# Kernel optimization log

Measured on AMD Instinct MI355X. Metric: run time of the kernel, lower is better.

The kernel has to match this reference:

```python
import jax, jax.numpy as jnp
import numpy as np
from jax import lax

ALPHA = 0.2                       # LeakyReLU leakage
BN_SCALE = 1.0 / np.sqrt(1.0 + 1e-3)  # inference-mode BN with default stats (mean=0, var=1, eps=1e-3)
COEFF = np.array([[-1., 3., -3., 1.],
                  [3., -6., 3., 0.],
                  [-3., 0., 3., 0.],
                  [1., 4., 1., 0.]], dtype=np.float32)


def _conv(x, w):
    return lax.conv_general_dilated(x, w, (1, 1), 'SAME',
                                    dimension_numbers=('NHWC', 'HWIO', 'NHWC'))


def _lrelu(x):
    return jnp.where(x > 0, x, ALPHA * x)


def _avgpool2(x):
    b, h, w, c = x.shape
    return x.reshape(b, h // 2, 2, w // 2, 2, c).mean(axis=(2, 4))


def _run_cnn(fixed, moving, ws, fw0, fw1, pw0, pw1):
    x = jnp.concatenate([fixed, moving], axis=-1)  # [B,H,W,2]
    for w in ws:
        x = _avgpool2(_lrelu(BN_SCALE * _conv(x, w)))
    x = _lrelu(BN_SCALE * _conv(x, fw0))
    x = _lrelu(BN_SCALE * _conv(x, fw1))
    x = _lrelu(_conv(x, pw0))
    return _conv(x, pw1)  # [B, H/2^s, W/2^s, 2] coarse displacements


def _range_grid(n, size):
    # mirrors __makeMeshgrids: step = 1/floor(size/n), clipped to [0, n-1]
    fd = size // n
    step = 1.0 / fd
    r = np.arange(0.0, n + step * (fd - 1), step)[:size]
    return np.clip(r, 0.0, n - 1).astype(np.float32)


def _bvec(t):
    return jnp.stack([t ** 3, t ** 2, t, jnp.ones_like(t)], axis=-1)


def _bspline_interp(disp, H, W):
    ny, nx = disp.shape[1], disp.shape[2]
    xr = _range_grid(nx, W)
    yr = _range_grid(ny, H)
    xx, yy = np.meshgrid(xr, yr)               # [H, W]
    ii = np.floor(xx).astype(np.int32)
    jj = np.floor(yy).astype(np.int32)
    u = jnp.asarray((xx / nx).astype(np.float32))
    v = jnp.asarray((yy / ny).astype(np.float32))
    padded = jnp.pad(disp, ((0, 0), (1, 3), (1, 3), (0, 0)))
    # G[m, n, b, h, w, c] = padded[b, jj+m, ii+n, c]  (m ~ add_j, n ~ add_i)
    G = jnp.stack([jnp.stack([padded[:, jj + m, ii + n, :] for n in range(4)], 0)
                   for m in range(4)], 0)
    B_u = jnp.einsum('hwk,kl->hwl', _bvec(u), jnp.asarray(COEFF))
    B_v = jnp.einsum('hwk,kl->hwl', _bvec(v), jnp.asarray(COEFF))
    # matches: interm_u = B_u . m-axis ; res = interm_u . B_v over n-axis
    return jnp.einsum('hwm,hwn,mnbhwc->bhwc', B_u, B_v, G)


def _bilinear(img, wx, wy, H, W):
    eps = 1e-5
    x0 = jnp.clip(jnp.floor(wx), 0, W - 1)
    x1 = jnp.clip(jnp.floor(wx) + 1, 0, W - 1)
    y0 = jnp.clip(jnp.floor(wy), 0, H - 1)
    y1 = jnp.clip(jnp.floor(wy) + 1, 0, H - 1)
    x0i = x0.astype(jnp.int32); x1i = x1.astype(jnp.int32)
    y0i = y0.astype(jnp.int32); y1i = y1.astype(jnp.int32)
    im = img[..., 0]                            # [B,H,W], channel 0 only
    b = jnp.arange(im.shape[0])[:, None, None]
    Q1 = im[b, y0i, x0i]
    Q2 = im[b, y1i, x0i]
    Q3 = im[b, y0i, x1i]
    Q4 = im[b, y1i, x1i]
    wxr = (x1 - wx) / (x1 - x0 + eps)
    wxl = (wx - x0) / (x1 - x0 + eps)
    R1 = wxr * Q1 + wxl * Q3
    R2 = wxr * Q2 + wxl * Q4
    out = (y1 - wy) / (y1 - y0 + eps) * R1 + (wy - y0) / (y1 - y0 + eps) * R2
    return out[..., None]                       # [B,H,W,1]


def _forward(fixed, moving, w0, w1, w2, fw0, fw1, pw0, pw1):
    B, H, W, _ = moving.shape
    disp = _run_cnn(fixed, moving, (w0, w1, w2), fw0, fw1, pw0, pw1)
    interp = _bspline_interp(disp, H, W)        # [B,H,W,2]
    gx, gy = np.meshgrid(np.arange(W, dtype=np.float32), np.arange(H, dtype=np.float32))
    wx = interp[..., 0] + gx                    # warped x coords
    wy = interp[..., 1] + gy                    # warped y coords
    warped = _bilinear(moving, wx, wy, H, W)
    warped_grid = jnp.stack([wx, wy], axis=1)   # [B,2,H,W]
    return warped, warped_grid


def setup_inputs() -> dict:
    key = jax.random.key(0)
    ks = jax.random.split(key, 9)
    B, H, W = 4, 512, 512
    s = 0.05
    return {
        'fixed':  jax.random.normal(ks[0], (B, H, W, 1), jnp.float32),
        'moving': jax.random.normal(ks[1], (B, H, W, 1), jnp.float32),
        'w0':  s * jax.random.normal(ks[2], (3, 3, 2, 32), jnp.float32),
        'w1':  s * jax.random.normal(ks[3], (3, 3, 32, 32), jnp.float32),
        'w2':  s * jax.random.normal(ks[4], (3, 3, 32, 32), jnp.float32),
        'fw0': s * jax.random.normal(ks[5], (3, 3, 32, 32), jnp.float32),
        'fw1': s * jax.random.normal(ks[6], (3, 3, 32, 32), jnp.float32),
        'pw0': s * jax.random.normal(ks[7], (1, 1, 32, 32), jnp.float32),
        'pw1': s * jax.random.normal(ks[8], (1, 1, 32, 2), jnp.float32),
    }


def reference(fixed, moving, w0, w1, w2, fw0, fw1, pw0, pw1):
    return _forward(fixed, moving, w0, w1, w2, fw0, fw1, pw0, pw1)
```

## Files before the change

kernel.cpp:

```cpp
#include <hip/hip_runtime.h>
#include <hip/hip_bf16.h>

typedef __hip_bfloat16 bf16;
typedef __attribute__((ext_vector_type(8))) short s8v;
typedef __attribute__((ext_vector_type(16))) float f16v;

#define BNS 0.9995003746877732f

__device__ __forceinline__ float lrelu(float x) { return x > 0.f ? x : 0.2f * x; }

struct b4 { bf16 a, b, c, d; };
__device__ __forceinline__ float4 load4(const bf16* p) {
    const b4 q = *reinterpret_cast<const b4*>(p);
    return make_float4(__bfloat162float(q.a), __bfloat162float(q.b),
                       __bfloat162float(q.c), __bfloat162float(q.d));
}

__global__ __launch_bounds__(256) void k_repack(const float* __restrict__ wa,
                                                const float* __restrict__ wb,
                                                const float* __restrict__ wc,
                                                const float* __restrict__ wd,
                                                const float* __restrict__ w0,
                                                bf16* __restrict__ wf)
{
    const int idx = blockIdx.x * 256 + threadIdx.x;
    if (idx < 36864) {
        const int layer = idx / 9216;
        const int r = idx - layer * 9216;
        const int j = r & 7;
        const int l = (r >> 3) & 63;
        const int t = r >> 9;
        const int k = t * 16 + ((l >> 5) << 3) + j;
        const int tap = k >> 5, ci = k & 31, co = l & 31;
        const float* W = layer == 0 ? wa : layer == 1 ? wb : layer == 2 ? wc : wd;
        wf[idx] = __float2bfloat16(W[(tap * 32 + ci) * 32 + co]);
    } else {
        const int r = idx - 36864;
        const int j = r & 7;
        const int l = (r >> 3) & 63;
        const int s = r >> 9;
        const int k = s * 16 + ((l >> 5) << 3) + j;
        const int co = l & 31;
        const float v = (k < 18) ? w0[(k >> 1) * 64 + (k & 1) * 32 + co] : 0.f;
        wf[idx] = __float2bfloat16(v);
    }
}

__global__ __launch_bounds__(256) void k_stage0_mfma(const float* __restrict__ fx,
                                                     const float* __restrict__ mv,
                                                     const bf16* __restrict__ wf,
                                                     bf16* __restrict__ out)
{
    __shared__ uint lds[180];
    const int tid  = threadIdx.x;
    const int lane = tid & 63;
    const int wv   = tid >> 6;
    const int x0 = blockIdx.x * 16;
    const int y0 = blockIdx.y * 8;
    const int b  = blockIdx.z;

    if (tid < 180) {
        const int row = tid / 18, col = tid - row * 18;
        const int gy = y0 - 1 + row, gx = x0 - 1 + col;
        float vf = 0.f, vm = 0.f;
        if ((unsigned)gy < 512u && (unsigned)gx < 512u) {
            const size_t idx = ((size_t)b * 512 + gy) * 512 + gx;
            vf = fx[idx]; vm = mv[idx];
        }
        union { bf16 h[2]; uint u; } pk;
        pk.h[0] = __float2bfloat16(vf);
        pk.h[1] = __float2bfloat16(vm);
        lds[tid] = pk.u;
    }
    __syncthreads();

    const int m  = lane & 31;
    const int h  = lane >> 5;
    const int dy = m >> 4;
    const int xx = m & 15;
    const int rbase = 2 * wv + dy;

    uint p[16];
#pragma unroll
    for (int i = 9; i < 16; ++i) p[i] = 0u;
#pragma unroll
    for (int ky = 0; ky < 3; ++ky)
#pragma unroll
        for (int kx = 0; kx < 3; ++kx)
            p[ky * 3 + kx] = lds[(rbase + ky) * 18 + xx + kx];

    f16v acc;
#pragma unroll
    for (int i = 0; i < 16; ++i) acc[i] = 0.f;

#pragma unroll
    for (int s = 0; s < 2; ++s) {
        union { uint u[4]; s8v v; } af;
#pragma unroll
        for (int q = 0; q < 4; ++q) af.u[q] = p[s * 8 + h * 4 + q];
        const s8v bfg = *reinterpret_cast<const s8v*>(&wf[(s * 64 + lane) * 8]);
        acc = __builtin_amdgcn_mfma_f32_32x32x16_bf16(af.v, bfg, acc, 0, 0, 0);
    }

    const int co = lane & 31;
    const int prow = blockIdx.y * 4 + wv;
#pragma unroll
    for (int q = 0; q < 4; ++q) {
        const int base = ((q & 1) << 1) + ((q >> 1) << 2);
        const float s = lrelu(BNS * acc[base])     + lrelu(BNS * acc[base + 1])
                      + lrelu(BNS * acc[base + 8]) + lrelu(BNS * acc[base + 9]);
        const int c = (q & 1) + 2 * h + ((q >> 1) << 2);
        out[(((size_t)b * 256 + prow) * 256 + (blockIdx.x * 8 + c)) * 32 + co] =
            __float2bfloat16(0.25f * s);
    }
}

template <bool POOL>
__global__ __launch_bounds__(256) void k_conv_mfma(const bf16* __restrict__ in,
                                                   const bf16* __restrict__ wf,
                                                   bf16* __restrict__ out,
                                                   int Hi, int Wi)
{
    __shared__ __align__(16) short lds[7200];
    const int tid  = threadIdx.x;
    const int lane = tid & 63;
    const int wv   = tid >> 6;
    const int x0 = blockIdx.x * 16;
    const int y0 = blockIdx.y * 8;
    const int b  = blockIdx.z;

    for (int i = tid; i < 1440; i += 256) {
        const int c4 = i & 7;
        const int p  = i >> 3;
        const int row = p / 18, col = p - row * 18;
        const int gy = y0 - 1 + row, gx = x0 - 1 + col;
        uint2 v = make_uint2(0u, 0u);
        if ((unsigned)gy < (unsigned)Hi && (unsigned)gx < (unsigned)Wi)
            v = *reinterpret_cast<const uint2*>(&in[(((size_t)b * Hi + gy) * Wi + gx) * 32 + c4 * 4]);
        *reinterpret_cast<uint2*>(&lds[p * 40 + c4 * 4]) = v;
    }
    __syncthreads();

    const int m  = lane & 31;
    const int h  = lane >> 5;
    const int dy = m >> 4;
    const int xx = m & 15;
    const int rbase = 2 * wv + dy;

    f16v acc;
#pragma unroll
    for (int i = 0; i < 16; ++i) acc[i] = 0.f;

#pragma unroll
    for (int t = 0; t < 18; ++t) {
        const int tap = t >> 1;
        const int ky = tap / 3, kx = tap % 3;
        const int ci_ofs = ((t & 1) << 4) + (h << 3);
        const s8v a = *reinterpret_cast<const s8v*>(
            &lds[((rbase + ky) * 18 + (xx + kx)) * 40 + ci_ofs]);
        const s8v bf = *reinterpret_cast<const s8v*>(&wf[(t * 64 + lane) * 8]);
        acc = __builtin_amdgcn_mfma_f32_32x32x16_bf16(a, bf, acc, 0, 0, 0);
    }

    const int co = lane & 31;
    if (POOL) {
        const int Ho = Hi >> 1, Wo = Wi >> 1;
        const int prow = blockIdx.y * 4 + wv;
#pragma unroll
        for (int q = 0; q < 4; ++q) {
            const int base = ((q & 1) << 1) + ((q >> 1) << 2);
            const float s = lrelu(BNS * acc[base])     + lrelu(BNS * acc[base + 1])
                          + lrelu(BNS * acc[base + 8]) + lrelu(BNS * acc[base + 9]);
            const int c = (q & 1) + 2 * h + ((q >> 1) << 2);
            out[(((size_t)b * Ho + prow) * Wo + (blockIdx.x * 8 + c)) * 32 + co] =
                __float2bfloat16(0.25f * s);
        }
    } else {
#pragma unroll
        for (int r = 0; r < 16; ++r) {
            const int mm = (r & 3) + ((r >> 2) << 3) + (h << 2);
            const int gy = y0 + 2 * wv + (mm >> 4);
            const int gx = x0 + (mm & 15);
            out[(((size_t)b * Hi + gy) * Wi + gx) * 32 + co] =
                __float2bfloat16(lrelu(BNS * acc[r]));
        }
    }
}

__global__ __launch_bounds__(256) void k_pw(const bf16* __restrict__ in,
                                            const float* __restrict__ pw0,
                                            const float* __restrict__ pw1,
                                            float* __restrict__ disp)
{
    __shared__ float w0t[1024];
    __shared__ float w1s[64];
    const int tid = threadIdx.x;
    for (int i = tid; i < 1024; i += 256) {
        const int ci = i >> 5, co = i & 31;
        w0t[co * 32 + ci] = pw0[i];
    }
    if (tid < 64) w1s[tid] = pw1[tid];
    __syncthreads();

    const int p = blockIdx.x * 256 + tid;
    float4 iv[8];
#pragma unroll
    for (int g = 0; g < 8; ++g)
        iv[g] = load4(&in[(size_t)p * 32 + g * 4]);

    float d0 = 0.f, d1 = 0.f;
#pragma unroll 4
    for (int co = 0; co < 32; ++co) {
        float s = 0.f;
#pragma unroll
        for (int g = 0; g < 8; ++g) {
            const float4 wv = *reinterpret_cast<const float4*>(&w0t[co * 32 + g * 4]);
            s += iv[g].x * wv.x + iv[g].y * wv.y + iv[g].z * wv.z + iv[g].w * wv.w;
        }
        const float p0 = lrelu(s);
        d0 += p0 * w1s[co * 2 + 0];
        d1 += p0 * w1s[co * 2 + 1];
    }
    disp[(size_t)p * 2 + 0] = d0;
    disp[(size_t)p * 2 + 1] = d1;
}

__global__ __launch_bounds__(256) void k_warp(const float* __restrict__ disp,
                                              const float* __restrict__ mv,
                                              float* __restrict__ out)
{
    const int idx = blockIdx.x * 256 + threadIdx.x;
    const int b = idx >> 18;
    const int h = (idx >> 9) & 511;
    const int w = idx & 511;

    const float xg = fminf(w * 0.125f, 63.0f);
    const float yg = fminf(h * 0.125f, 63.0f);
    const int ii = w >> 3, jj = h >> 3;
    const float u = xg * 0.015625f, v = yg * 0.015625f;

    const float u2 = u * u, u3 = u2 * u;
    const float v2 = v * v, v3 = v2 * v;
    const float Bu[4] = {-u3 + 3.f * u2 - 3.f * u + 1.f,
                         3.f * u3 - 6.f * u2 + 4.f,
                         -3.f * u3 + 3.f * u2 + 3.f * u + 1.f,
                         u3};
    const float Bv[4] = {-v3 + 3.f * v2 - 3.f * v + 1.f,
                         3.f * v3 - 6.f * v2 + 4.f,
                         -3.f * v3 + 3.f * v2 + 3.f * v + 1.f,
                         v3};

    float s0 = 0.f, s1 = 0.f;
#pragma unroll
    for (int m = 0; m < 4; ++m) {
        const int gy = jj + m - 1;
        float r0 = 0.f, r1 = 0.f;
        if ((unsigned)gy < 64u) {
#pragma unroll
            for (int n = 0; n < 4; ++n) {
                const int gx = ii + n - 1;
                if ((unsigned)gx < 64u) {
                    const size_t di = (((size_t)b * 64 + gy) * 64 + gx) * 2;
                    r0 += Bv[n] * disp[di];
                    r1 += Bv[n] * disp[di + 1];
                }
            }
        }
        s0 += Bu[m] * r0;
        s1 += Bu[m] * r1;
    }
    const float wx = s0 + (float)w;
    const float wy = s1 + (float)h;

    const float fx = floorf(wx), fy = floorf(wy);
    const float x0 = fminf(fmaxf(fx, 0.f), 511.f);
    const float x1 = fminf(fmaxf(fx + 1.f, 0.f), 511.f);
    const float y0 = fminf(fmaxf(fy, 0.f), 511.f);
    const float y1 = fminf(fmaxf(fy + 1.f, 0.f), 511.f);
    const int x0i = (int)x0, x1i = (int)x1, y0i = (int)y0, y1i = (int)y1;

    float ov;
    if (x0i == x1i || y0i == y1i) {
        ov = 0.f;
    } else {
        const size_t bb = (size_t)b * 262144;
        const float Q1 = mv[bb + (size_t)y0i * 512 + x0i];
        const float Q2 = mv[bb + (size_t)y1i * 512 + x0i];
        const float Q3 = mv[bb + (size_t)y0i * 512 + x1i];
        const float Q4 = mv[bb + (size_t)y1i * 512 + x1i];
        const float invdx = 1.f / (x1 - x0 + 1e-5f);
        const float wxr = (x1 - wx) * invdx, wxl = (wx - x0) * invdx;
        const float R1 = wxr * Q1 + wxl * Q3;
        const float R2 = wxr * Q2 + wxl * Q4;
        const float invdy = 1.f / (y1 - y0 + 1e-5f);
        ov = (y1 - wy) * invdy * R1 + (wy - y0) * invdy * R2;
    }

    out[idx] = ov;
    const size_t gbase = 1048576;
    out[gbase + (size_t)(b * 2 + 0) * 262144 + (size_t)h * 512 + w] = wx;
    out[gbase + (size_t)(b * 2 + 1) * 262144 + (size_t)h * 512 + w] = wy;
}

extern "C" void kernel_launch(void* const* d_in, const int* in_sizes, int n_in,
                              void* d_out, int out_size, void* d_ws, size_t ws_size,
                              hipStream_t stream) {
    (void)in_sizes; (void)n_in; (void)out_size; (void)ws_size;
    const float* fixed  = (const float*)d_in[0];
    const float* moving = (const float*)d_in[1];
    const float* w0  = (const float*)d_in[2];
    const float* w1  = (const float*)d_in[3];
    const float* w2  = (const float*)d_in[4];
    const float* fw0 = (const float*)d_in[5];
    const float* fw1 = (const float*)d_in[6];
    const float* pw0 = (const float*)d_in[7];
    const float* pw1 = (const float*)d_in[8];

    char* base = (char*)d_ws;
    bf16*  a0  = (bf16*)base;
    bf16*  a1  = (bf16*)(base + (16u << 20));
    bf16*  a2  = (bf16*)base;
    bf16*  f0  = (bf16*)(base + (1u << 20));
    bf16*  f1  = (bf16*)(base + (2u << 20));
    float* dsp = (float*)(base + (3u << 20));
    bf16*  wfr = (bf16*)d_out;

    k_repack<<<148, 256, 0, stream>>>(w1, w2, fw0, fw1, w0, wfr);
    k_stage0_mfma<<<dim3(32, 64, 4), 256, 0, stream>>>(fixed, moving, wfr + 36864, a0);
    k_conv_mfma<true ><<<dim3(16, 32, 4), 256, 0, stream>>>(a0, wfr + 0 * 9216, a1, 256, 256);
    k_conv_mfma<true ><<<dim3( 8, 16, 4), 256, 0, stream>>>(a1, wfr + 1 * 9216, a2, 128, 128);
    k_conv_mfma<false><<<dim3( 4,  8, 4), 256, 0, stream>>>(a2, wfr + 2 * 9216, f0,  64,  64);
    k_conv_mfma<false><<<dim3( 4,  8, 4), 256, 0, stream>>>(f0, wfr + 3 * 9216, f1,  64,  64);
    k_pw<<<64, 256, 0, stream>>>(f1, pw0, pw1, dsp);
    k_warp<<<4096, 256, 0, stream>>>(dsp, moving, (float*)d_out);
}
```

Measured before the change: 146.6 us.

## Fuse conv stages into front and tail kernels with halo recompute in LDS

Merges stage-0 conv with the first pooled conv into one kernel that computes the 256x256 intermediate tile (with halo) in shared memory, skipping the global round-trip of the largest activation. Also fuses the two 64x64 convs, the pointwise head, and the B-spline warp into a single tail kernel that keeps per-tile displacements in LDS. Launch count drops from eight to four. In exchange, halo regions are recomputed redundantly, and the tail runs only 256 blocks with heavy LDS use, which may limit occupancy.

```diff
diff --git a/kernel.cpp b/kernel.cpp
--- a/kernel.cpp
+++ b/kernel.cpp
@@ -14,6 +14,25 @@
     const b4 q = *reinterpret_cast<const b4*>(p);
     return make_float4(__bfloat162float(q.a), __bfloat162float(q.b),
                        __bfloat162float(q.c), __bfloat162float(q.d));
+}
+
+__device__ __forceinline__ f16v conv18(const short* lds, int ldw, int pi, int pj,
+                                       int h, const bf16* __restrict__ wf, int lane)
+{
+    f16v acc;
+#pragma unroll
+    for (int i = 0; i < 16; ++i) acc[i] = 0.f;
+#pragma unroll
+    for (int t = 0; t < 18; ++t) {
+        const int tap = t >> 1;
+        const int ky = tap / 3, kx = tap % 3;
+        const int ci_ofs = ((t & 1) << 4) + (h << 3);
+        const s8v a = *reinterpret_cast<const s8v*>(
+            &lds[((pi + ky) * ldw + (pj + kx)) * 40 + ci_ofs]);
+        const s8v bfg = *reinterpret_cast<const s8v*>(&wf[(t * 64 + lane) * 8]);
+        acc = __builtin_amdgcn_mfma_f32_32x32x16_bf16(a, bfg, acc, 0, 0, 0);
+    }
+    return acc;
 }
 
 __global__ __launch_bounds__(256) void k_repack(const float* __restrict__ wa,
@@ -46,63 +65,83 @@
     }
 }
 
-__global__ __launch_bounds__(256) void k_stage0_mfma(const float* __restrict__ fx,
-                                                     const float* __restrict__ mv,
-                                                     const bf16* __restrict__ wf,
-                                                     bf16* __restrict__ out)
+__global__ __launch_bounds__(256) void k_front(const float* __restrict__ fx,
+                                               const float* __restrict__ mv,
+                                               const bf16* __restrict__ wfs0,
+                                               const bf16* __restrict__ wfc1,
+                                               bf16* __restrict__ a1)
 {
-    __shared__ uint lds[180];
+    __shared__ uint rawL[864];
+    __shared__ __align__(16) short a0L[7200];
     const int tid  = threadIdx.x;
     const int lane = tid & 63;
     const int wv   = tid >> 6;
+    const int h  = lane >> 5;
+    const int m  = lane & 31;
+    const int dy = m >> 4;
+    const int xx = m & 15;
     const int x0 = blockIdx.x * 16;
     const int y0 = blockIdx.y * 8;
     const int b  = blockIdx.z;
-
-    if (tid < 180) {
-        const int row = tid / 18, col = tid - row * 18;
-        const int gy = y0 - 1 + row, gx = x0 - 1 + col;
-        float vf = 0.f, vm = 0.f;
-        if ((unsigned)gy < 512u && (unsigned)gx < 512u) {
-            const size_t idx = ((size_t)b * 512 + gy) * 512 + gx;
-            vf = fx[idx]; vm = mv[idx];
-        }
-        union { bf16 h[2]; uint u; } pk;
-        pk.h[0] = __float2bfloat16(vf);
-        pk.h[1] = __float2bfloat16(vm);
-        lds[tid] = pk.u;
-    }
-    __syncthreads();
-
-    const int m  = lane & 31;
-    const int h  = lane >> 5;
-    const int dy = m >> 4;
-    const int xx = m & 15;
-    const int rbase = 2 * wv + dy;
-
-    uint p[16];
-#pragma unroll
-    for (int i = 9; i < 16; ++i) p[i] = 0u;
-#pragma unroll
-    for (int ky = 0; ky < 3; ++ky)
-#pragma unroll
-        for (int kx = 0; kx < 3; ++kx)
-            p[ky * 3 + kx] = lds[(rbase + ky) * 18 + xx + kx];
-
-    f16v acc;
-#pragma unroll
-    for (int i = 0; i < 16; ++i) acc[i] = 0.f;
-
-#pragma unroll
-    for (int s = 0; s < 2; ++s) {
-        union { uint u[4]; s8v v; } af;
-#pragma unroll
-        for (int q = 0; q < 4; ++q) af.u[q] = p[s * 8 + h * 4 + q];
-        const s8v bfg = *reinterpret_cast<const s8v*>(&wf[(s * 64 + lane) * 8]);
-        acc = __builtin_amdgcn_mfma_f32_32x32x16_bf16(af.v, bfg, acc, 0, 0, 0);
-    }
-
     const int co = lane & 31;
+
+    for (int i = tid; i < 864; i += 256) {
+        uint pk = 0u;
+        if (i < 836) {
+            const int row = i / 38, col = i - (i / 38) * 38;
+            const int gy = 2 * y0 - 3 + row, gx = 2 * x0 - 3 + col;
+            if ((unsigned)gy < 512u && (unsigned)gx < 512u) {
+                const size_t idx = ((size_t)b * 512 + gy) * 512 + gx;
+                union { bf16 hh[2]; uint u; } p;
+                p.hh[0] = __float2bfloat16(fx[idx]);
+                p.hh[1] = __float2bfloat16(mv[idx]);
+                pk = p.u;
+            }
+        }
+        rawL[i] = pk;
+    }
+    __syncthreads();
+
+    const s8v b0 = *reinterpret_cast<const s8v*>(&wfs0[(0 * 64 + lane) * 8]);
+    const s8v b1 = *reinterpret_cast<const s8v*>(&wfs0[(1 * 64 + lane) * 8]);
+    for (int T = wv; T < 30; T += 4) {
+        const int r = T / 3, g = T - 3 * r;
+        const int pr = 2 * r + dy, pc = g * 16 + xx;
+        uint p[9];
+#pragma unroll
+        for (int ky = 0; ky < 3; ++ky)
+#pragma unroll
+            for (int kx = 0; kx < 3; ++kx)
+                p[ky * 3 + kx] = rawL[(pr + ky) * 38 + pc + kx];
+
+        f16v acc;
+#pragma unroll
+        for (int i = 0; i < 16; ++i) acc[i] = 0.f;
+        union { uint u[4]; s8v v; } a0f, a1f;
+#pragma unroll
+        for (int q = 0; q < 4; ++q) a0f.u[q] = p[h * 4 + q];
+        a1f.u[0] = (h == 0) ? p[8] : 0u;
+        a1f.u[1] = 0u; a1f.u[2] = 0u; a1f.u[3] = 0u;
+        acc = __builtin_amdgcn_mfma_f32_32x32x16_bf16(a0f.v, b0, acc, 0, 0, 0);
+        acc = __builtin_amdgcn_mfma_f32_32x32x16_bf16(a1f.v, b1, acc, 0, 0, 0);
+
+#pragma unroll
+        for (int q = 0; q < 4; ++q) {
+            const int base = ((q & 1) << 1) + ((q >> 1) << 2);
+            const float s = lrelu(BNS * acc[base])     + lrelu(BNS * acc[base + 1])
+                          + lrelu(BNS * acc[base + 8]) + lrelu(BNS * acc[base + 9]);
+            const int col = g * 8 + ((q & 1) + 2 * h + ((q >> 1) << 2));
+            if (col < 18) {
+                const int gy0 = y0 - 1 + r, gx0 = x0 - 1 + col;
+                const float val = ((unsigned)gy0 < 256u && (unsigned)gx0 < 256u)
+                                  ? 0.25f * s : 0.f;
+                a0L[(r * 18 + col) * 40 + co] = __float2bfloat16(val);
+            }
+        }
+    }
+    __syncthreads();
+
+    const f16v acc = conv18(a0L, 18, 2 * wv + dy, xx, h, wfc1, lane);
     const int prow = blockIdx.y * 4 + wv;
 #pragma unroll
     for (int q = 0; q < 4; ++q) {
@@ -110,16 +149,15 @@
         const float s = lrelu(BNS * acc[base])     + lrelu(BNS * acc[base + 1])
                       + lrelu(BNS * acc[base + 8]) + lrelu(BNS * acc[base + 9]);
         const int c = (q & 1) + 2 * h + ((q >> 1) << 2);
-        out[(((size_t)b * 256 + prow) * 256 + (blockIdx.x * 8 + c)) * 32 + co] =
+        a1[(((size_t)b * 128 + prow) * 128 + (blockIdx.x * 8 + c)) * 32 + co] =
             __float2bfloat16(0.25f * s);
     }
 }
 
-template <bool POOL>
-__global__ __launch_bounds__(256) void k_conv_mfma(const bf16* __restrict__ in,
-                                                   const bf16* __restrict__ wf,
-                                                   bf16* __restrict__ out,
-                                                   int Hi, int Wi)
+__global__ __launch_bounds__(256) void k_conv2(const bf16* __restrict__ in,
+                                               const bf16* __restrict__ wf,
+                                               bf16* __restrict__ out,
+                                               int Hi, int Wi)
 {
     __shared__ __align__(16) short lds[7200];
     const int tid  = threadIdx.x;
@@ -145,161 +183,197 @@
     const int h  = lane >> 5;
     const int dy = m >> 4;
     const int xx = m & 15;
-    const int rbase = 2 * wv + dy;
-
-    f16v acc;
-#pragma unroll
-    for (int i = 0; i < 16; ++i) acc[i] = 0.f;
-
-#pragma unroll
-    for (int t = 0; t < 18; ++t) {
-        const int tap = t >> 1;
-        const int ky = tap / 3, kx = tap % 3;
-        const int ci_ofs = ((t & 1) << 4) + (h << 3);
-        const s8v a = *reinterpret_cast<const s8v*>(
-            &lds[((rbase + ky) * 18 + (xx + kx)) * 40 + ci_ofs]);
-        const s8v bf = *reinterpret_cast<const s8v*>(&wf[(t * 64 + lane) * 8]);
-        acc = __builtin_amdgcn_mfma_f32_32x32x16_bf16(a, bf, acc, 0, 0, 0);
-    }
+
+    const f16v acc = conv18(lds, 18, 2 * wv + dy, xx, h, wf, lane);
 
     const int co = lane & 31;
-    if (POOL) {
-        const int Ho = Hi >> 1, Wo = Wi >> 1;
-        const int prow = blockIdx.y * 4 + wv;
-#pragma unroll
-        for (int q = 0; q < 4; ++q) {
-            const int base = ((q & 1) << 1) + ((q >> 1) << 2);
-            const float s = lrelu(BNS * acc[base])     + lrelu(BNS * acc[base + 1])
-                          + lrelu(BNS * acc[base + 8]) + lrelu(BNS * acc[base + 9]);
-            const int c = (q & 1) + 2 * h + ((q >> 1) << 2);
-            out[(((size_t)b * Ho + prow) * Wo + (blockIdx.x * 8 + c)) * 32 + co] =
-                __float2bfloat16(0.25f * s);
-        }
-    } else {
-#pragma unroll
-        for (int r = 0; r < 16; ++r) {
-            const int mm = (r & 3) + ((r >> 2) << 3) + (h << 2);
-            const int gy = y0 + 2 * wv + (mm >> 4);
-            const int gx = x0 + (mm & 15);
-            out[(((size_t)b * Hi + gy) * Wi + gx) * 32 + co] =
-                __float2bfloat16(lrelu(BNS * acc[r]));
-        }
-    }
-}
-
-__global__ __launch_bounds__(256) void k_pw(const bf16* __restrict__ in,
-                                            const float* __restrict__ pw0,
-                                            const float* __restrict__ pw1,
-                                            float* __restrict__ disp)
-{
-    __shared__ float w0t[1024];
-    __shared__ float w1s[64];
-    const int tid = threadIdx.x;
-    for (int i = tid; i < 1024; i += 256) {
-        const int ci = i >> 5, co = i & 31;
-        w0t[co * 32 + ci] = pw0[i];
-    }
-    if (tid < 64) w1s[tid] = pw1[tid];
-    __syncthreads();
-
-    const int p = blockIdx.x * 256 + tid;
-    float4 iv[8];
-#pragma unroll
-    for (int g = 0; g < 8; ++g)
-        iv[g] = load4(&in[(size_t)p * 32 + g * 4]);
-
-    float d0 = 0.f, d1 = 0.f;
-#pragma unroll 4
-    for (int co = 0; co < 32; ++co) {
-        float s = 0.f;
-#pragma unroll
-        for (int g = 0; g < 8; ++g) {
-            const float4 wv = *reinterpret_cast<const float4*>(&w0t[co * 32 + g * 4]);
-            s += iv[g].x * wv.x + iv[g].y * wv.y + iv[g].z * wv.z + iv[g].w * wv.w;
-        }
-        const float p0 = lrelu(s);
-        d0 += p0 * w1s[co * 2 + 0];
-        d1 += p0 * w1s[co * 2 + 1];
-    }
-    disp[(size_t)p * 2 + 0] = d0;
-    disp[(size_t)p * 2 + 1] = d1;
-}
-
-__global__ __launch_bounds__(256) void k_warp(const float* __restrict__ disp,
+    const int Ho = Hi >> 1, Wo = Wi >> 1;
+    const int prow = blockIdx.y * 4 + wv;
+#pragma unroll
+    for (int q = 0; q < 4; ++q) {
+        const int base = ((q & 1) << 1) + ((q >> 1) << 2);
+        const float s = lrelu(BNS * acc[base])     + lrelu(BNS * acc[base + 1])
+                      + lrelu(BNS * acc[base + 8]) + lrelu(BNS * acc[base + 9]);
+        const int c = (q & 1) + 2 * h + ((q >> 1) << 2);
+        out[(((size_t)b * Ho + prow) * Wo + (blockIdx.x * 8 + c)) * 32 + co] =
+            __float2bfloat16(0.25f * s);
+    }
+}
+
+__global__ __launch_bounds__(256) void k_tail(const bf16* __restrict__ a2,
+                                              const bf16* __restrict__ wf2,
+                                              const bf16* __restrict__ wf3,
+                                              const float* __restrict__ pw0,
+                                              const float* __restrict__ pw1,
                                               const float* __restrict__ mv,
                                               float* __restrict__ out)
 {
-    const int idx = blockIdx.x * 256 + threadIdx.x;
-    const int b = idx >> 18;
-    const int h = (idx >> 9) & 511;
-    const int w = idx & 511;
-
-    const float xg = fminf(w * 0.125f, 63.0f);
-    const float yg = fminf(h * 0.125f, 63.0f);
-    const int ii = w >> 3, jj = h >> 3;
-    const float u = xg * 0.015625f, v = yg * 0.015625f;
-
-    const float u2 = u * u, u3 = u2 * u;
-    const float v2 = v * v, v3 = v2 * v;
-    const float Bu[4] = {-u3 + 3.f * u2 - 3.f * u + 1.f,
-                         3.f * u3 - 6.f * u2 + 4.f,
-                         -3.f * u3 + 3.f * u2 + 3.f * u + 1.f,
-                         u3};
-    const float Bv[4] = {-v3 + 3.f * v2 - 3.f * v + 1.f,
-                         3.f * v3 - 6.f * v2 + 4.f,
-                         -3.f * v3 + 3.f * v2 + 3.f * v + 1.f,
-                         v3};
-
-    float s0 = 0.f, s1 = 0.f;
-#pragma unroll
-    for (int m = 0; m < 4; ++m) {
-        const int gy = jj + m - 1;
-        float r0 = 0.f, r1 = 0.f;
-        if ((unsigned)gy < 64u) {
-#pragma unroll
-            for (int n = 0; n < 4; ++n) {
-                const int gx = ii + n - 1;
-                if ((unsigned)gx < 64u) {
-                    const size_t di = (((size_t)b * 64 + gy) * 64 + gx) * 2;
-                    r0 += Bv[n] * disp[di];
-                    r1 += Bv[n] * disp[di + 1];
+    __shared__ __align__(16) short a2L[288 * 40];
+    __shared__ __align__(16) short f0L[252 * 40];
+    __shared__ __align__(16) short f1L[121 * 40];
+    __shared__ float dspL[121 * 2];
+    __shared__ float w0t[1024];
+    __shared__ float w1s[64];
+
+    const int tid  = threadIdx.x;
+    const int lane = tid & 63;
+    const int wv   = tid >> 6;
+    const int h  = lane >> 5;
+    const int dy = (lane & 31) >> 4;
+    const int xx = lane & 15;
+    const int co = lane & 31;
+    const int bx = blockIdx.x, by = blockIdx.y, b = blockIdx.z;
+    const int Dy = by * 8 - 1, Dx = bx * 8 - 1;
+
+    for (int i = tid; i < 2304; i += 256) {
+        const int c4 = i & 7;
+        const int p  = i >> 3;
+        const int row = p / 18, col = p - row * 18;
+        const int gy = Dy - 2 + row, gx = Dx - 2 + col;
+        uint2 v = make_uint2(0u, 0u);
+        if (row < 15 && col < 15 && (unsigned)gy < 64u && (unsigned)gx < 64u)
+            v = *reinterpret_cast<const uint2*>(&a2[(((size_t)b * 64 + gy) * 64 + gx) * 32 + c4 * 4]);
+        *reinterpret_cast<uint2*>(&a2L[p * 40 + c4 * 4]) = v;
+    }
+    for (int i = tid; i < 560; i += 256) {
+        const int p28 = i / 20, w = i - (i / 20) * 20;
+        const int row = p28 >> 1, col = 16 + (p28 & 1);
+        reinterpret_cast<uint*>(f0L)[(row * 18 + col) * 20 + w] = 0u;
+    }
+    for (int i = tid; i < 1024; i += 256) {
+        const int ci = i >> 5, c = i & 31;
+        w0t[c * 32 + ci] = pw0[i];
+    }
+    if (tid < 64) w1s[tid] = pw1[tid];
+    __syncthreads();
+
+    for (int T = wv; T < 7; T += 4) {
+        const f16v acc = conv18(a2L, 18, 2 * T + dy, xx, h, wf2, lane);
+#pragma unroll
+        for (int r = 0; r < 16; ++r) {
+            const int row32 = (r & 3) + ((r >> 2) << 3) + (h << 2);
+            const int i = 2 * T + (row32 >> 4);
+            const int j = row32 & 15;
+            const int gy = Dy - 1 + i, gx = Dx - 1 + j;
+            const float val = (i < 13 && j < 13 &&
+                               (unsigned)gy < 64u && (unsigned)gx < 64u)
+                              ? lrelu(BNS * acc[r]) : 0.f;
+            f0L[(i * 18 + j) * 40 + co] = __float2bfloat16(val);
+        }
+    }
+    __syncthreads();
+
+    for (int T = wv; T < 6; T += 4) {
+        const f16v acc = conv18(f0L, 18, 2 * T + dy, xx, h, wf3, lane);
+#pragma unroll
+        for (int r = 0; r < 16; ++r) {
+            const int row32 = (r & 3) + ((r >> 2) << 3) + (h << 2);
+            const int i = 2 * T + (row32 >> 4);
+            const int j = row32 & 15;
+            if (i < 11 && j < 11)
+                f1L[(i * 11 + j) * 40 + co] = __float2bfloat16(lrelu(BNS * acc[r]));
+        }
+    }
+    __syncthreads();
+
+    if (tid < 121) {
+        const int i = tid / 11, j = tid - (tid / 11) * 11;
+        const int gy = Dy + i, gx = Dx + j;
+        float d0 = 0.f, d1 = 0.f;
+        if ((unsigned)gy < 64u && (unsigned)gx < 64u) {
+            float4 iv[8];
+#pragma unroll
+            for (int g = 0; g < 8; ++g)
+                iv[g] = load4(reinterpret_cast<const bf16*>(&f1L[tid * 40 + g * 4]));
+#pragma unroll 4
+            for (int c = 0; c < 32; ++c) {
+                float s = 0.f;
+#pragma unroll
+                for (int g = 0; g < 8; ++g) {
+                    const float4 wvv = *reinterpret_cast<const float4*>(&w0t[c * 32 + g * 4]);
+                    s += iv[g].x * wvv.x + iv[g].y * wvv.y + iv[g].z * wvv.z + iv[g].w * wvv.w;
                 }
+                const float p0 = lrelu(s);
+                d0 += p0 * w1s[c * 2 + 0];
+                d1 += p0 * w1s[c * 2 + 1];
             }
         }
-        s0 += Bu[m] * r0;
-        s1 += Bu[m] * r1;
-    }
-    const float wx = s0 + (float)w;
-    const float wy = s1 + (float)h;
-
-    const float fx = floorf(wx), fy = floorf(wy);
-    const float x0 = fminf(fmaxf(fx, 0.f), 511.f);
-    const float x1 = fminf(fmaxf(fx + 1.f, 0.f), 511.f);
-    const float y0 = fminf(fmaxf(fy, 0.f), 511.f);
-    const float y1 = fminf(fmaxf(fy + 1.f, 0.f), 511.f);
-    const int x0i = (int)x0, x1i = (int)x1, y0i = (int)y0, y1i = (int)y1;
-
-    float ov;
-    if (x0i == x1i || y0i == y1i) {
-        ov = 0.f;
-    } else {
-        const size_t bb = (size_t)b * 262144;
-        const float Q1 = mv[bb + (size_t)y0i * 512 + x0i];
-        const float Q2 = mv[bb + (size_t)y1i * 512 + x0i];
-        const float Q3 = mv[bb + (size_t)y0i * 512 + x1i];
-        const float Q4 = mv[bb + (size_t)y1i * 512 + x1i];
-        const float invdx = 1.f / (x1 - x0 + 1e-5f);
-        const float wxr = (x1 - wx) * invdx, wxl = (wx - x0) * invdx;
-        const float R1 = wxr * Q1 + wxl * Q3;
-        const float R2 = wxr * Q2 + wxl * Q4;
-        const float invdy = 1.f / (y1 - y0 + 1e-5f);
-        ov = (y1 - wy) * invdy * R1 + (wy - y0) * invdy * R2;
-    }
-
-    out[idx] = ov;
-    const size_t gbase = 1048576;
-    out[gbase + (size_t)(b * 2 + 0) * 262144 + (size_t)h * 512 + w] = wx;
-    out[gbase + (size_t)(b * 2 + 1) * 262144 + (size_t)h * 512 + w] = wy;
+        dspL[tid * 2 + 0] = d0;
+        dspL[tid * 2 + 1] = d1;
+    }
+    __syncthreads();
+
+    const int hy = by * 64, hx = bx * 64;
+#pragma unroll 2
+    for (int k = 0; k < 16; ++k) {
+        const int l = k * 256 + tid;
+        const int hh = hy + (l >> 6);
+        const int ww = hx + (l & 63);
+
+        const float xg = fminf(ww * 0.125f, 63.0f);
+        const float yg = fminf(hh * 0.125f, 63.0f);
+        const float u = xg * 0.015625f, v = yg * 0.015625f;
+        const int lr = (hh >> 3) - by * 8 + 1;
+        const int lc = (ww >> 3) - bx * 8 + 1;
+
+        const float u2 = u * u, u3 = u2 * u;
+        const float v2 = v * v, v3 = v2 * v;
+        const float Bu[4] = {-u3 + 3.f * u2 - 3.f * u + 1.f,
+                             3.f * u3 - 6.f * u2 + 4.f,
+                             -3.f * u3 + 3.f * u2 + 3.f * u + 1.f,
+                             u3};
+        const float Bv[4] = {-v3 + 3.f * v2 - 3.f * v + 1.f,
+                             3.f * v3 - 6.f * v2 + 4.f,
+                             -3.f * v3 + 3.f * v2 + 3.f * v + 1.f,
+                             v3};
+
+        float s0 = 0.f, s1 = 0.f;
+#pragma unroll
+        for (int mm = 0; mm < 4; ++mm) {
+            const int row = lr + mm - 1;
+            float r0 = 0.f, r1 = 0.f;
+#pragma unroll
+            for (int nn = 0; nn < 4; ++nn) {
+                const int col = lc + nn - 1;
+                const float2 d = *reinterpret_cast<const float2*>(&dspL[(row * 11 + col) * 2]);
+                r0 += Bv[nn] * d.x;
+                r1 += Bv[nn] * d.y;
+            }
+            s0 += Bu[mm] * r0;
+            s1 += Bu[mm] * r1;
+        }
+        const float wx = s0 + (float)ww;
+        const float wy = s1 + (float)hh;
+
+        const float fxx = floorf(wx), fyy = floorf(wy);
+        const float x0 = fminf(fmaxf(fxx, 0.f), 511.f);
+        const float x1 = fminf(fmaxf(fxx + 1.f, 0.f), 511.f);
+        const float y0 = fminf(fmaxf(fyy, 0.f), 511.f);
+        const float y1 = fminf(fmaxf(fyy + 1.f, 0.f), 511.f);
+        const int x0i = (int)x0, x1i = (int)x1, y0i = (int)y0, y1i = (int)y1;
+
+        float ov;
+        if (x0i == x1i || y0i == y1i) {
+            ov = 0.f;
+        } else {
+            const size_t bb = (size_t)b * 262144;
+            const float Q1 = mv[bb + (size_t)y0i * 512 + x0i];
+            const float Q2 = mv[bb + (size_t)y1i * 512 + x0i];
+            const float Q3 = mv[bb + (size_t)y0i * 512 + x1i];
+            const float Q4 = mv[bb + (size_t)y1i * 512 + x1i];
+            const float invdx = 1.f / (x1 - x0 + 1e-5f);
+            const float wxr = (x1 - wx) * invdx, wxl = (wx - x0) * invdx;
+            const float R1 = wxr * Q1 + wxl * Q3;
+            const float R2 = wxr * Q2 + wxl * Q4;
+            const float invdy = 1.f / (y1 - y0 + 1e-5f);
+            ov = (y1 - wy) * invdy * R1 + (wy - y0) * invdy * R2;
+        }
+
+        const size_t pix = (size_t)hh * 512 + ww;
+        out[(size_t)b * 262144 + pix] = ov;
+        out[1048576 + (size_t)(b * 2 + 0) * 262144 + pix] = wx;
+        out[1048576 + (size_t)(b * 2 + 1) * 262144 + pix] = wy;
+    }
 }
 
 extern "C" void kernel_launch(void* const* d_in, const int* in_sizes, int n_in,
@@ -317,20 +391,14 @@
     const float* pw1 = (const float*)d_in[8];
 
     char* base = (char*)d_ws;
-    bf16*  a0  = (bf16*)base;
-    bf16*  a1  = (bf16*)(base + (16u << 20));
-    bf16*  a2  = (bf16*)base;
-    bf16*  f0  = (bf16*)(base + (1u << 20));
-    bf16*  f1  = (bf16*)(base + (2u << 20));
-    float* dsp = (float*)(base + (3u << 20));
-    bf16*  wfr = (bf16*)d_out;
+    bf16* wfr = (bf16*)base;
+    bf16* a1  = (bf16*)(base + (1u << 20));
+    bf16* a2  = (bf16*)(base + (6u << 20));
 
     k_repack<<<148, 256, 0, stream>>>(w1, w2, fw0, fw1, w0, wfr);
-    k_stage0_mfma<<<dim3(32, 64, 4), 256, 0, stream>>>(fixed, moving, wfr + 36864, a0);
-    k_conv_mfma<true ><<<dim3(16, 32, 4), 256, 0, stream>>>(a0, wfr + 0 * 9216, a1, 256, 256);
-    k_conv_mfma<true ><<<dim3( 8, 16, 4), 256, 0, stream>>>(a1, wfr + 1 * 9216, a2, 128, 128);
-    k_conv_mfma<false><<<dim3( 4,  8, 4), 256, 0, stream>>>(a2, wfr + 2 * 9216, f0,  64,  64);
-    k_conv_mfma<false><<<dim3( 4,  8, 4), 256, 0, stream>>>(f0, wfr + 3 * 9216, f1,  64,  64);
-    k_pw<<<64, 256, 0, stream>>>(f1, pw0, pw1, dsp);
-    k_warp<<<4096, 256, 0, stream>>>(dsp, moving, (float*)d_out);
-}
+    k_front<<<dim3(16, 32, 4), 256, 0, stream>>>(fixed, moving,
+                                                 wfr + 36864, wfr + 0 * 9216, a1);
+    k_conv2<<<dim3(8, 16, 4), 256, 0, stream>>>(a1, wfr + 1 * 9216, a2, 128, 128);
+    k_tail<<<dim3(8, 8, 4), 256, 0, stream>>>(a2, wfr + 2 * 9216, wfr + 3 * 9216,
+                                              pw0, pw1, moving, (float*)d_out);
+}
```

Result: faster. 132.6 us (-9.6%).
